# Kernel tuning notes

Measured on AMD Instinct MI355X. Metric: run time of the kernel, lower is better.

## Reference

```python
import jax, jax.numpy as jnp
import numpy as np

N = 50000          # nodes
E = 800000         # edges (avg degree 16)
HID = 128          # hidden_dim
NUM_RBF = 32
CUTOFF = 6.0
LIGAND_NODE = 0
D_IN = 3 * HID + NUM_RBF + 1  # 417


def setup_inputs() -> dict:
    key = jax.random.key(0)
    ks = jax.random.split(key, 16)
    s = 0.05
    return {
        "h": jax.random.normal(ks[0], (N, HID), dtype=jnp.float32),
        "pos": jax.random.normal(ks[1], (N, 3), dtype=jnp.float32) * 3.0,
        "edge_index": jax.random.randint(ks[2], (2, E), 0, N, dtype=jnp.int32),
        "edge_type": jax.random.randint(ks[3], (E,), 0, 2, dtype=jnp.int32),
        "node_type": jax.random.randint(ks[4], (N,), 0, 2, dtype=jnp.int32),
        "emb": jax.random.normal(ks[5], (2, HID), dtype=jnp.float32) * s,
        "mw1": jax.random.normal(ks[6], (D_IN, HID), dtype=jnp.float32) * s,
        "mb1": jnp.zeros((HID,), dtype=jnp.float32),
        "mw2": jax.random.normal(ks[7], (HID, HID), dtype=jnp.float32) * s,
        "mb2": jnp.zeros((HID,), dtype=jnp.float32),
        "uw1": jax.random.normal(ks[8], (2 * HID, HID), dtype=jnp.float32) * s,
        "ub1": jnp.zeros((HID,), dtype=jnp.float32),
        "uw2": jax.random.normal(ks[9], (HID, HID), dtype=jnp.float32) * s,
        "ub2": jnp.zeros((HID,), dtype=jnp.float32),
        "ln_g": jnp.ones((HID,), dtype=jnp.float32),
        "ln_b": jnp.zeros((HID,), dtype=jnp.float32),
    }


def _silu(x):
    return x * jax.nn.sigmoid(x)


def _layernorm(x, g, b, eps=1e-5):
    mu = jnp.mean(x, axis=-1, keepdims=True)
    var = jnp.var(x, axis=-1, keepdims=True)
    return (x - mu) * jax.lax.rsqrt(var + eps) * g + b


def reference(h, pos, edge_index, edge_type, node_type,
              emb, mw1, mb1, mw2, mb2, uw1, ub1, uw2, ub2, ln_g, ln_b):
    # Gaussian RBF setup (matches torch.linspace(0, cutoff, num_rbf))
    centers = jnp.linspace(0.0, CUTOFF, NUM_RBF)          # [R]
    step = CUTOFF / (NUM_RBF - 1)
    gamma = 1.0 / max(step * step, 1e-6)

    src, dst = edge_index[0], edge_index[1]               # [E]
    rel = pos[src] - pos[dst]                             # [E,3]
    dist = jnp.linalg.norm(rel, axis=-1)                  # [E]
    radial = jnp.exp(-gamma * (dist[:, None] - centers[None, :]) ** 2)  # [E,R]
    edge_kind = emb[edge_type]                            # [E,H]

    # edge message MLP (dropout in eval mode = identity)
    m_in = jnp.concatenate([h[src], h[dst], edge_kind, radial, dist[:, None]], axis=-1)  # [E, 3H+R+1]
    x = _silu(m_in @ mw1 + mb1)
    messages = _silu(x @ mw2 + mb2)                       # [E,H]

    # scatter-mean over dst into N nodes
    sums = jax.ops.segment_sum(messages, dst, num_segments=N)           # [N,H]
    counts = jax.ops.segment_sum(jnp.ones((E,), dtype=h.dtype), dst, num_segments=N)
    aggregated = sums / jnp.maximum(counts, 1.0)[:, None]

    # node update MLP
    u = _silu(jnp.concatenate([h, aggregated], axis=-1) @ uw1 + ub1)
    update = u @ uw2 + ub2                                # [N,H]

    # masked residual + LayerNorm (only ligand nodes updated)
    normed = _layernorm(h + update, ln_g, ln_b)
    ligand_mask = (node_type == LIGAND_NODE)[:, None]
    return jnp.where(ligand_mask, normed, h)
```

## Files before the change

kernel.cpp:

```cpp
#include <hip/hip_runtime.h>
#include <hip/hip_bf16.h>
#include <math.h>

#define NN   50000
#define NE   800000
#define HID  128
#define NRBF 32
#define NSCAN_BLOCKS ((NN + 255) / 256)

typedef __attribute__((ext_vector_type(8))) short short8;
typedef __attribute__((ext_vector_type(4))) float floatx4;

constexpr int TILE_N = 64;

__device__ __forceinline__ float silu_f(float x) {
  return x / (1.0f + __expf(-x));
}
__device__ __forceinline__ ushort f2bf(float f) {
  __hip_bfloat16 b = __float2bfloat16(f);
  return *reinterpret_cast<ushort*>(&b);
}
__device__ __forceinline__ float bf2f(ushort u) {
  union { uint u32; float f; } c; c.u32 = ((uint)u) << 16; return c.f;
}

__global__ void counts_i_kernel(const int* __restrict__ edge_index, int* __restrict__ cnt) {
  const int e = blockIdx.x * blockDim.x + threadIdx.x;
  if (e < NE) atomicAdd(&cnt[edge_index[NE + e]], 1);
}

__global__ void scan_a_kernel(const int* __restrict__ cnt, int* __restrict__ incl,
                              int* __restrict__ bsum) {
  __shared__ int s[256];
  const int i = blockIdx.x * 256 + threadIdx.x;
  const int v = (i < NN) ? cnt[i] : 0;
  s[threadIdx.x] = v;
  __syncthreads();
  for (int off = 1; off < 256; off <<= 1) {
    const int x = (threadIdx.x >= off) ? s[threadIdx.x - off] : 0;
    __syncthreads();
    s[threadIdx.x] += x;
    __syncthreads();
  }
  if (i < NN) incl[i] = s[threadIdx.x];
  if (threadIdx.x == 255) bsum[blockIdx.x] = s[255];
}

__global__ void scan_b_kernel(int* __restrict__ bsum, int nb) {
  __shared__ int s[256];
  const int v = (threadIdx.x < nb) ? bsum[threadIdx.x] : 0;
  s[threadIdx.x] = v;
  __syncthreads();
  for (int off = 1; off < 256; off <<= 1) {
    const int x = (threadIdx.x >= off) ? s[threadIdx.x - off] : 0;
    __syncthreads();
    s[threadIdx.x] += x;
    __syncthreads();
  }
  bsum[threadIdx.x] = s[threadIdx.x] - v;
}

__global__ void scan_c_kernel(int* __restrict__ incl, const int* __restrict__ cnt,
                              const int* __restrict__ bsumex, float* __restrict__ cf) {
  const int i = blockIdx.x * 256 + threadIdx.x;
  if (i < NN) {
    const int c = cnt[i];
    incl[i] = incl[i] - c + bsumex[blockIdx.x];
    cf[i] = (float)c;
  }
}

__global__ void perm_kernel(const int* __restrict__ edge_index, const int* __restrict__ edge_type,
                            const int* __restrict__ starts,
                            int* __restrict__ cursor, int2* __restrict__ rec) {
  const int e = blockIdx.x * blockDim.x + threadIdx.x;
  if (e < NE) {
    const int s  = edge_index[e];
    const int d  = edge_index[NE + e];
    const int et = edge_type[e];
    const int pos = atomicAdd(&cursor[d], 1);
    rec[starts[d] + pos] = make_int2(s | (et << 24), d);
  }
}

__global__ void embp_kernel(const float* __restrict__ emb, const float* __restrict__ mw1,
                            const float* __restrict__ mb1, float* __restrict__ embp) {
  const int t = threadIdx.x;
  const int row = t >> 7, col = t & 127;
  float s = mb1[col];
  #pragma unroll 4
  for (int k = 0; k < HID; ++k)
    s = fmaf(emb[row * HID + k], mw1[(256 + k) * HID + col], s);
  embp[row * HID + col] = s;
}

__global__ void pack_w_kernel(const float* __restrict__ W, ushort* __restrict__ out,
                              int Korig, int nks) {
  const int tid = blockIdx.x * blockDim.x + threadIdx.x;
  if (tid >= nks * 8 * 64) return;
  const int l = tid & 63;
  const int c = (tid >> 6) & 7;
  const int kk = tid >> 9;
  union { ushort u[8]; uint4 v; } o;
  #pragma unroll
  for (int j = 0; j < 8; ++j) {
    const int k = kk * 32 + ((l >> 4) * 8) + j;
    const float f = (k < Korig) ? W[k * HID + c * 16 + (l & 15)] : 0.0f;
    o.u[j] = f2bf(f);
  }
  reinterpret_cast<uint4*>(out)[tid] = o.v;
}

__global__ __launch_bounds__(256, 3)
void proj_kernel(const float* __restrict__ h,
                 const ushort* __restrict__ wap, const ushort* __restrict__ wbp,
                 ushort* __restrict__ hs_proj, ushort* __restrict__ hd_proj)
{
  __shared__ __align__(16) ushort sH[64 * HID];
  char* const sHb = reinterpret_cast<char*>(sH);
  const int t  = threadIdx.x;
  const int n0 = blockIdx.x * 64;

  {
    const int e = t >> 2, c0 = (t & 3) * 32;
    const int node = n0 + e;
    const int sm = (e & 7) << 4;
    #pragma unroll
    for (int m = 0; m < 4; ++m) {
      const int c = c0 + m * 8;
      float4 f0 = make_float4(0,0,0,0), f1 = f0;
      if (node < NN) {
        f0 = *reinterpret_cast<const float4*>(h + (long)node * HID + c);
        f1 = *reinterpret_cast<const float4*>(h + (long)node * HID + c + 4);
      }
      union { ushort u[8]; uint4 v; } o;
      o.u[0]=f2bf(f0.x); o.u[1]=f2bf(f0.y); o.u[2]=f2bf(f0.z); o.u[3]=f2bf(f0.w);
      o.u[4]=f2bf(f1.x); o.u[5]=f2bf(f1.y); o.u[6]=f2bf(f1.z); o.u[7]=f2bf(f1.w);
      *reinterpret_cast<uint4*>(sHb + ((e * 256 + c * 2) ^ sm)) = o.v;
    }
  }
  __syncthreads();

  const int lane = t & 63;
  const int w    = t >> 6;
  const int rt0  = (w & 1) * 2;
  const int ct0  = (w >> 1) * 4;
  const int lrow = lane & 15;
  const int lk16 = (lane >> 4) * 16;
  const int rowA0 = rt0 * 16 + lrow, rowA1 = rowA0 + 16;
  const int smA0 = (rowA0 & 7) << 4, smA1 = (rowA1 & 7) << 4;

  floatx4 accA[2][4] = {}, accB[2][4] = {};
  const ushort* const baseA = wap + ((size_t)ct0 * 64 + lane) * 8;
  const ushort* const baseB = wbp + ((size_t)ct0 * 64 + lane) * 8;
  #pragma unroll
  for (int kk = 0; kk < 4; ++kk) {
    short8 afr[2];
    afr[0] = *reinterpret_cast<const short8*>(sHb + rowA0 * 256 + ((kk*64 + lk16) ^ smA0));
    afr[1] = *reinterpret_cast<const short8*>(sHb + rowA1 * 256 + ((kk*64 + lk16) ^ smA1));
    #pragma unroll
    for (int j = 0; j < 4; ++j) {
      const short8 bA = *reinterpret_cast<const short8*>(baseA + kk * 4096 + j * 512);
      const short8 bB = *reinterpret_cast<const short8*>(baseB + kk * 4096 + j * 512);
      #pragma unroll
      for (int i = 0; i < 2; ++i) {
        accA[i][j] = __builtin_amdgcn_mfma_f32_16x16x32_bf16(afr[i], bA, accA[i][j], 0, 0, 0);
        accB[i][j] = __builtin_amdgcn_mfma_f32_16x16x32_bf16(afr[i], bB, accB[i][j], 0, 0, 0);
      }
    }
  }
  #pragma unroll
  for (int i = 0; i < 2; ++i)
    #pragma unroll
    for (int r = 0; r < 4; ++r) {
      const int row = (rt0 + i) * 16 + (lane >> 4) * 4 + r;
      const int node = n0 + row;
      if (node < NN) {
        #pragma unroll
        for (int j = 0; j < 4; ++j) {
          const int col = (ct0 + j) * 16 + lrow;
          hs_proj[(long)node * HID + col] = f2bf(accA[i][j][r]);
          hd_proj[(long)node * HID + col] = f2bf(accB[i][j][r]);
        }
      }
    }
}

__global__ __launch_bounds__(256, 4)
void edge_kernel(const ushort* __restrict__ hs_proj, const ushort* __restrict__ hd_proj,
                 const float* __restrict__ pos, const int2* __restrict__ rec,
                 const float* __restrict__ embp, const float* __restrict__ w416,
                 const ushort* __restrict__ w1dp, const ushort* __restrict__ w2p,
                 const float* __restrict__ mb2,
                 float* sums)
{
  __shared__ __align__(16) uint4 sRbf[64 * 4];
  __shared__ __align__(16) char  sBuf[64 * 512];
  __shared__ int sDst[64];

  const int t  = threadIdx.x;
  const int e0 = blockIdx.x * 64;
  const int e  = t >> 2, q = t & 3;

  const int2 rc = rec[e0 + e];
  const int src = rc.x & 0x00FFFFFF;
  const int et  = ((unsigned)rc.x) >> 24;
  const int dst = rc.y;
  if (q == 0) sDst[e] = dst;

  const float dx = pos[3*src]   - pos[3*dst];
  const float dy = pos[3*src+1] - pos[3*dst+1];
  const float dz = pos[3*src+2] - pos[3*dst+2];
  const float dist = sqrtf(dx*dx + dy*dy + dz*dz);

  {
    const int c0 = q * 32;
    const ushort* const hsr = hs_proj + (long)src * HID;
    const ushort* const hdr = hd_proj + (long)dst * HID;
    const float*  const ep  = embp + et * HID;
    const int sm = (e & 7) << 4;
    #pragma unroll
    for (int m = 0; m < 4; ++m) {
      const int c = c0 + m * 8;
      const uint4 a = *reinterpret_cast<const uint4*>(hsr + c);
      const uint4 b = *reinterpret_cast<const uint4*>(hdr + c);
      const float4 ef0 = *reinterpret_cast<const float4*>(ep + c);
      const float4 ef1 = *reinterpret_cast<const float4*>(ep + c + 4);
      const float4 w0  = *reinterpret_cast<const float4*>(w416 + c);
      const float4 w1  = *reinterpret_cast<const float4*>(w416 + c + 4);
      const ushort* au = reinterpret_cast<const ushort*>(&a);
      const ushort* bu = reinterpret_cast<const ushort*>(&b);
      float4 o0, o1;
      o0.x = bf2f(au[0]) + bf2f(bu[0]) + ef0.x + dist * w0.x;
      o0.y = bf2f(au[1]) + bf2f(bu[1]) + ef0.y + dist * w0.y;
      o0.z = bf2f(au[2]) + bf2f(bu[2]) + ef0.z + dist * w0.z;
      o0.w = bf2f(au[3]) + bf2f(bu[3]) + ef0.w + dist * w0.w;
      o1.x = bf2f(au[4]) + bf2f(bu[4]) + ef1.x + dist * w1.x;
      o1.y = bf2f(au[5]) + bf2f(bu[5]) + ef1.y + dist * w1.y;
      o1.z = bf2f(au[6]) + bf2f(bu[6]) + ef1.z + dist * w1.z;
      o1.w = bf2f(au[7]) + bf2f(bu[7]) + ef1.w + dist * w1.w;
      const int byte0 = e * 512 + c * 4;
      *reinterpret_cast<float4*>(sBuf + (byte0 ^ sm))        = o0;
      *reinterpret_cast<float4*>(sBuf + ((byte0 + 16) ^ sm)) = o1;
    }
    const float step  = 6.0f / 31.0f;
    const float gamma = 1.0f / (step * step);
    const int r0 = q * 8;
    union { ushort u[8]; uint4 v; } o;
    #pragma unroll
    for (int j = 0; j < 8; ++j) {
      const float dd = dist - step * (float)(r0 + j);
      o.u[j] = f2bf(__expf(-gamma * dd * dd));
    }
    sRbf[e * 4 + (q ^ (e & 3))] = o.v;
  }
  __syncthreads();

  const int lane = t & 63;
  const int w    = t >> 6;
  const int rt0  = (w & 1) * 2;
  const int ct0  = (w >> 1) * 4;
  const int lrow = lane & 15;
  const int lk16 = (lane >> 4) * 16;
  const int rowA0 = rt0 * 16 + lrow, rowA1 = rowA0 + 16;
  const int smA0 = (rowA0 & 7) << 4, smA1 = (rowA1 & 7) << 4;

  floatx4 acc[2][4];
  #pragma unroll
  for (int i = 0; i < 2; ++i)
    #pragma unroll
    for (int r = 0; r < 4; ++r) {
      const int row = (rt0 + i) * 16 + (lane >> 4) * 4 + r;
      const int sm = (row & 7) << 4;
      #pragma unroll
      for (int j = 0; j < 4; ++j) {
        const int col = (ct0 + j) * 16 + lrow;
        acc[i][j][r] = *reinterpret_cast<const float*>(sBuf + ((row * 512 + col * 4) ^ sm));
      }
    }
  {
    short8 a0 = *reinterpret_cast<const short8*>(&sRbf[rowA0 * 4 + ((lane >> 4) ^ (rowA0 & 3))]);
    short8 a1 = *reinterpret_cast<const short8*>(&sRbf[rowA1 * 4 + ((lane >> 4) ^ (rowA1 & 3))]);
    #pragma unroll
    for (int j = 0; j < 4; ++j) {
      const short8 b = *reinterpret_cast<const short8*>(w1dp + ((size_t)(ct0 + j) * 64 + lane) * 8);
      acc[0][j] = __builtin_amdgcn_mfma_f32_16x16x32_bf16(a0, b, acc[0][j], 0, 0, 0);
      acc[1][j] = __builtin_amdgcn_mfma_f32_16x16x32_bf16(a1, b, acc[1][j], 0, 0, 0);
    }
  }
  __syncthreads();

  #pragma unroll
  for (int i = 0; i < 2; ++i)
    #pragma unroll
    for (int r = 0; r < 4; ++r) {
      const int row = (rt0 + i) * 16 + (lane >> 4) * 4 + r;
      const int sm = (row & 7) << 4;
      #pragma unroll
      for (int j = 0; j < 4; ++j) {
        const int col = (ct0 + j) * 16 + lrow;
        *reinterpret_cast<ushort*>(sBuf + row * 256 + ((col * 2) ^ sm)) = f2bf(silu_f(acc[i][j][r]));
      }
    }
  __syncthreads();

  floatx4 acc2[2][4] = {};
  {
    const ushort* const bbase = w2p + ((size_t)ct0 * 64 + lane) * 8;
    #pragma unroll 2
    for (int kk = 0; kk < 4; ++kk) {
      short8 bfr[4];
      #pragma unroll
      for (int j = 0; j < 4; ++j)
        bfr[j] = *reinterpret_cast<const short8*>(bbase + kk * 4096 + j * 512);
      short8 afr[2];
      afr[0] = *reinterpret_cast<const short8*>(sBuf + rowA0 * 256 + ((kk*64 + lk16) ^ smA0));
      afr[1] = *reinterpret_cast<const short8*>(sBuf + rowA1 * 256 + ((kk*64 + lk16) ^ smA1));
      #pragma unroll
      for (int i = 0; i < 2; ++i)
        #pragma unroll
        for (int j = 0; j < 4; ++j)
          acc2[i][j] = __builtin_amdgcn_mfma_f32_16x16x32_bf16(afr[i], bfr[j], acc2[i][j], 0, 0, 0);
    }
  }
  __syncthreads();

  {
    float b2v[4];
    #pragma unroll
    for (int j = 0; j < 4; ++j) b2v[j] = mb2[(ct0 + j) * 16 + lrow];
    #pragma unroll
    for (int i = 0; i < 2; ++i)
      #pragma unroll
      for (int r = 0; r < 4; ++r) {
        const int row = (rt0 + i) * 16 + (lane >> 4) * 4 + r;
        const int sm = (row & 7) << 4;
        #pragma unroll
        for (int j = 0; j < 4; ++j) {
          const int col = (ct0 + j) * 16 + lrow;
          *reinterpret_cast<float*>(sBuf + ((row * 512 + col * 4) ^ sm)) =
              silu_f(acc2[i][j][r] + b2v[j]);
        }
      }
  }
  __syncthreads();

  {
    const int half = t >> 7;
    const int c    = t & 127;
    const int r0   = half * 32;
    int cur = sDst[r0];
    float accv = 0.0f;
    for (int r = r0; r < r0 + 32; ++r) {
      const int d = sDst[r];
      const float mv = *reinterpret_cast<const float*>(
          sBuf + ((r * 512 + c * 4) ^ ((r & 7) << 4)));
      if (d != cur) {
        atomicAdd(&sums[(long)cur * HID + c], accv);
        accv = 0.0f;
        cur = d;
      }
      accv += mv;
    }
    atomicAdd(&sums[(long)cur * HID + c], accv);
  }
}

__global__ __launch_bounds__(256, 2)
void node_kernel(const float* __restrict__ h,
                 const float* sums, const float* __restrict__ counts,
                 const int* __restrict__ node_type,
                 const float* __restrict__ uw1, const float* __restrict__ ub1,
                 const float* __restrict__ uw2, const float* __restrict__ ub2,
                 const float* __restrict__ ln_g, const float* __restrict__ ln_b,
                 float* out)
{
  __shared__ float sIn[TILE_N * 256];
  __shared__ float sMu[TILE_N];
  __shared__ float sRs[TILE_N];

  const int t  = threadIdx.x;
  const int n0 = blockIdx.x * TILE_N;

  for (int idx = t; idx < TILE_N*HID; idx += 256) {
    const int n = idx >> 7, c = idx & (HID-1);
    const int node = n0 + n;
    float hv = 0.f, av = 0.f;
    if (node < NN) {
      hv = h[(long)node*HID + c];
      av = sums[(long)node*HID + c] / fmaxf(counts[node], 1.0f);
    }
    sIn[n*256 + c]       = hv;
    sIn[n*256 + HID + c] = av;
  }
  __syncthreads();

  const int tx = t & 31;
  const int ty = t >> 5;

  const float* wp = uw1 + tx*4;
  float4 acc[8];
  #pragma unroll
  for (int i = 0; i < 8; ++i) acc[i] = make_float4(0.f,0.f,0.f,0.f);
  for (int k = 0; k < 2*HID; ++k) {
    const float4 w = *reinterpret_cast<const float4*>(wp + (long)k*HID);
    #pragma unroll
    for (int i = 0; i < 8; ++i) {
      const float a = sIn[(ty*8+i)*256 + k];
      acc[i].x = fmaf(a, w.x, acc[i].x);
      acc[i].y = fmaf(a, w.y, acc[i].y);
      acc[i].z = fmaf(a, w.z, acc[i].z);
      acc[i].w = fmaf(a, w.w, acc[i].w);
    }
  }
  __syncthreads();

  const float4 b1 = *reinterpret_cast<const float4*>(ub1 + tx*4);
  #pragma unroll
  for (int i = 0; i < 8; ++i) {
    const int e = ty*8 + i;
    float4 v = acc[i];
    v.x = silu_f(v.x + b1.x); v.y = silu_f(v.y + b1.y);
    v.z = silu_f(v.z + b1.z); v.w = silu_f(v.w + b1.w);
    *reinterpret_cast<float4*>(&sIn[e*256 + HID + tx*4]) = v;
  }
  __syncthreads();

  const float* wp2 = uw2 + tx*4;
  float4 acc2[8];
  #pragma unroll
  for (int i = 0; i < 8; ++i) acc2[i] = make_float4(0.f,0.f,0.f,0.f);
  for (int k = 0; k < HID; ++k) {
    const float4 w = *reinterpret_cast<const float4*>(wp2 + (long)k*HID);
    #pragma unroll
    for (int i = 0; i < 8; ++i) {
      const float a = sIn[(ty*8+i)*256 + HID + k];
      acc2[i].x = fmaf(a, w.x, acc2[i].x);
      acc2[i].y = fmaf(a, w.y, acc2[i].y);
      acc2[i].z = fmaf(a, w.z, acc2[i].z);
      acc2[i].w = fmaf(a, w.w, acc2[i].w);
    }
  }
  __syncthreads();

  const float4 b2 = *reinterpret_cast<const float4*>(ub2 + tx*4);
  #pragma unroll
  for (int i = 0; i < 8; ++i) {
    const int e = ty*8 + i;
    float4 v = acc2[i];
    v.x = sIn[e*256 + tx*4+0] + v.x + b2.x;
    v.y = sIn[e*256 + tx*4+1] + v.y + b2.y;
    v.z = sIn[e*256 + tx*4+2] + v.z + b2.z;
    v.w = sIn[e*256 + tx*4+3] + v.w + b2.w;
    *reinterpret_cast<float4*>(&sIn[e*256 + HID + tx*4]) = v;
  }
  __syncthreads();

  {
    const int n = t >> 2, q = t & 3;
    float sm = 0.f, sq = 0.f;
    #pragma unroll 8
    for (int i = 0; i < 32; ++i) {
      const float v = sIn[n*256 + HID + q*32 + i];
      sm += v; sq += v*v;
    }
    sm += __shfl_xor(sm, 1); sq += __shfl_xor(sq, 1);
    sm += __shfl_xor(sm, 2); sq += __shfl_xor(sq, 2);
    const float mu  = sm * (1.0f/HID);
    float var = sq * (1.0f/HID) - mu*mu;
    var = fmaxf(var, 0.0f);
    if (q == 0) { sMu[n] = mu; sRs[n] = rsqrtf(var + 1e-5f); }
  }
  __syncthreads();

  for (int idx = t; idx < TILE_N*HID; idx += 256) {
    const int n = idx >> 7, c = idx & (HID-1);
    const int node = n0 + n;
    if (node >= NN) continue;
    const float xv = sIn[n*256 + HID + c];
    const float normed = (xv - sMu[n]) * sRs[n] * ln_g[c] + ln_b[c];
    const float hv = sIn[n*256 + c];
    out[(long)node*HID + c] = (node_type[node] == 0) ? normed : hv;
  }
}

extern "C" void kernel_launch(void* const* d_in, const int* in_sizes, int n_in,
                              void* d_out, int out_size, void* d_ws, size_t ws_size,
                              hipStream_t stream)
{
  const float* h    = (const float*)d_in[0];
  const float* pos  = (const float*)d_in[1];
  const int*   eidx = (const int*)  d_in[2];
  const int*   etyp = (const int*)  d_in[3];
  const int*   ntyp = (const int*)  d_in[4];
  const float* emb  = (const float*)d_in[5];
  const float* mw1  = (const float*)d_in[6];
  const float* mb1  = (const float*)d_in[7];
  const float* mw2  = (const float*)d_in[8];
  const float* mb2  = (const float*)d_in[9];
  const float* uw1  = (const float*)d_in[10];
  const float* ub1  = (const float*)d_in[11];
  const float* uw2  = (const float*)d_in[12];
  const float* ub2  = (const float*)d_in[13];
  const float* lng  = (const float*)d_in[14];
  const float* lnb  = (const float*)d_in[15];

  float* sums = (float*)d_out;

  float*  counts_f = (float*)d_ws;
  ushort* hs_proj  = (ushort*)(counts_f + NN);
  ushort* hd_proj  = hs_proj + (long)NN*HID;
  float*  embp     = (float*)(hd_proj + (long)NN*HID);
  ushort* wap      = (ushort*)(embp + 256);
  ushort* wbp      = wap + 4*4096;
  ushort* w1dp     = wbp + 4*4096;
  ushort* w2p      = w1dp + 1*4096;
  int*    cnt_i    = (int*)(w2p + 4*4096);
  int*    cursor   = cnt_i + NN;
  int*    starts   = cursor + NN;
  int*    bsum     = starts + NN;
  int2*   rec      = (int2*)(bsum + 256);

  hipMemsetAsync(sums, 0, (size_t)NN*HID*4, stream);
  hipMemsetAsync(cnt_i, 0, (size_t)NN*2*4, stream);

  counts_i_kernel<<<(NE + 255)/256, 256, 0, stream>>>(eidx, cnt_i);
  scan_a_kernel<<<NSCAN_BLOCKS, 256, 0, stream>>>(cnt_i, starts, bsum);
  scan_b_kernel<<<1, 256, 0, stream>>>(bsum, NSCAN_BLOCKS);
  scan_c_kernel<<<NSCAN_BLOCKS, 256, 0, stream>>>(starts, cnt_i, bsum, counts_f);
  perm_kernel<<<(NE + 255)/256, 256, 0, stream>>>(eidx, etyp, starts, cursor, rec);

  embp_kernel<<<1, 256, 0, stream>>>(emb, mw1, mb1, embp);
  pack_w_kernel<<<8,  256, 0, stream>>>(mw1,             wap,  128, 4);
  pack_w_kernel<<<8,  256, 0, stream>>>(mw1 + 128*HID,   wbp,  128, 4);
  pack_w_kernel<<<2,  256, 0, stream>>>(mw1 + 384*HID,   w1dp,  32, 1);
  pack_w_kernel<<<8,  256, 0, stream>>>(mw2,             w2p,  128, 4);

  proj_kernel<<<(NN + 63)/64, 256, 0, stream>>>(h, wap, wbp, hs_proj, hd_proj);
  edge_kernel<<<NE/64, 256, 0, stream>>>(hs_proj, hd_proj, pos, rec,
                                         embp, mw1 + 416*HID, w1dp, w2p, mb2, sums);
  node_kernel<<<(NN + 63)/64, 256, 0, stream>>>(h, sums, counts_f, ntyp,
                                                uw1, ub1, uw2, ub2,
                                                lng, lnb, (float*)d_out);
}
```

Before: 447.5 us.

## Shrink edge kernel LDS via bf16 staging and fold dist/embedding terms into MFMA

The edge kernel now stages the summed projections and the final messages in shared memory as bf16 instead of fp32, which cuts LDS from about 49KB to about 20KB per block. Launch bounds rise from 4 to 7 blocks per CU. The dist*w416 and edge-type embedding contributions are moved out of per-element FMAs and into an extra K=32 MFMA step, using one-hot edge-type columns and a packed extra weight block built by a new prep kernel. In exchange, precision drops from rounding the pre-activation sums, dist and the messages to bf16, and there is one extra MFMA pass per tile.

Measured after the change: 533.4 us. 19.2% more time.

```diff
diff --git a/kernel.cpp b/kernel.cpp
--- a/kernel.cpp
+++ b/kernel.cpp
@@ -94,6 +94,19 @@
   embp[row * HID + col] = s;
 }
 
+__global__ void build_w1x_kernel(const float* __restrict__ mw1, const float* __restrict__ embp,
+                                 float* __restrict__ w1x) {
+  const int tid = blockIdx.x * 256 + threadIdx.x;
+  if (tid >= 64 * 128) return;
+  const int r = tid >> 7, c = tid & 127;
+  float v = 0.0f;
+  if (r < 32)       v = mw1[(384 + r) * HID + c];
+  else if (r == 32) v = mw1[416 * HID + c];
+  else if (r == 33) v = embp[c];
+  else if (r == 34) v = embp[HID + c];
+  w1x[tid] = v;
+}
+
 __global__ void pack_w_kernel(const float* __restrict__ W, ushort* __restrict__ out,
                               int Korig, int nks) {
   const int tid = blockIdx.x * blockDim.x + threadIdx.x;
@@ -186,17 +199,17 @@
     }
 }
 
-__global__ __launch_bounds__(256, 4)
+__global__ __launch_bounds__(256, 7)
 void edge_kernel(const ushort* __restrict__ hs_proj, const ushort* __restrict__ hd_proj,
                  const float* __restrict__ pos, const int2* __restrict__ rec,
-                 const float* __restrict__ embp, const float* __restrict__ w416,
-                 const ushort* __restrict__ w1dp, const ushort* __restrict__ w2p,
+                 const ushort* __restrict__ w1xp, const ushort* __restrict__ w2p,
                  const float* __restrict__ mb2,
                  float* sums)
 {
-  __shared__ __align__(16) uint4 sRbf[64 * 4];
-  __shared__ __align__(16) char  sBuf[64 * 512];
-  __shared__ int sDst[64];
+  __shared__ __align__(16) char sBuf[20480];
+  __shared__ int   sDst[64];
+  __shared__ int   sEt[64];
+  __shared__ float sDistF[64];
 
   const int t  = threadIdx.x;
   const int e0 = blockIdx.x * 64;
@@ -206,42 +219,28 @@
   const int src = rc.x & 0x00FFFFFF;
   const int et  = ((unsigned)rc.x) >> 24;
   const int dst = rc.y;
-  if (q == 0) sDst[e] = dst;
 
   const float dx = pos[3*src]   - pos[3*dst];
   const float dy = pos[3*src+1] - pos[3*dst+1];
   const float dz = pos[3*src+2] - pos[3*dst+2];
   const float dist = sqrtf(dx*dx + dy*dy + dz*dz);
-
-  {
-    const int c0 = q * 32;
+  if (q == 0) { sDst[e] = dst; sEt[e] = et; sDistF[e] = dist; }
+
+  {
     const ushort* const hsr = hs_proj + (long)src * HID;
     const ushort* const hdr = hd_proj + (long)dst * HID;
-    const float*  const ep  = embp + et * HID;
     const int sm = (e & 7) << 4;
     #pragma unroll
     for (int m = 0; m < 4; ++m) {
-      const int c = c0 + m * 8;
+      const int c = q * 32 + m * 8;
       const uint4 a = *reinterpret_cast<const uint4*>(hsr + c);
       const uint4 b = *reinterpret_cast<const uint4*>(hdr + c);
-      const float4 ef0 = *reinterpret_cast<const float4*>(ep + c);
-      const float4 ef1 = *reinterpret_cast<const float4*>(ep + c + 4);
-      const float4 w0  = *reinterpret_cast<const float4*>(w416 + c);
-      const float4 w1  = *reinterpret_cast<const float4*>(w416 + c + 4);
       const ushort* au = reinterpret_cast<const ushort*>(&a);
       const ushort* bu = reinterpret_cast<const ushort*>(&b);
-      float4 o0, o1;
-      o0.x = bf2f(au[0]) + bf2f(bu[0]) + ef0.x + dist * w0.x;
-      o0.y = bf2f(au[1]) + bf2f(bu[1]) + ef0.y + dist * w0.y;
-      o0.z = bf2f(au[2]) + bf2f(bu[2]) + ef0.z + dist * w0.z;
-      o0.w = bf2f(au[3]) + bf2f(bu[3]) + ef0.w + dist * w0.w;
-      o1.x = bf2f(au[4]) + bf2f(bu[4]) + ef1.x + dist * w1.x;
-      o1.y = bf2f(au[5]) + bf2f(bu[5]) + ef1.y + dist * w1.y;
-      o1.z = bf2f(au[6]) + bf2f(bu[6]) + ef1.z + dist * w1.z;
-      o1.w = bf2f(au[7]) + bf2f(bu[7]) + ef1.w + dist * w1.w;
-      const int byte0 = e * 512 + c * 4;
-      *reinterpret_cast<float4*>(sBuf + (byte0 ^ sm))        = o0;
-      *reinterpret_cast<float4*>(sBuf + ((byte0 + 16) ^ sm)) = o1;
+      union { ushort u[8]; uint4 v; } o;
+      #pragma unroll
+      for (int j = 0; j < 8; ++j) o.u[j] = f2bf(bf2f(au[j]) + bf2f(bu[j]));
+      *reinterpret_cast<uint4*>(sBuf + ((e * 256 + c * 2) ^ sm)) = o.v;
     }
     const float step  = 6.0f / 31.0f;
     const float gamma = 1.0f / (step * step);
@@ -252,7 +251,7 @@
       const float dd = dist - step * (float)(r0 + j);
       o.u[j] = f2bf(__expf(-gamma * dd * dd));
     }
-    sRbf[e * 4 + (q ^ (e & 3))] = o.v;
+    reinterpret_cast<uint4*>(sBuf + 16384)[e * 4 + (q ^ (e & 3))] = o.v;
   }
   __syncthreads();
 
@@ -275,20 +274,37 @@
       #pragma unroll
       for (int j = 0; j < 4; ++j) {
         const int col = (ct0 + j) * 16 + lrow;
-        acc[i][j][r] = *reinterpret_cast<const float*>(sBuf + ((row * 512 + col * 4) ^ sm));
-      }
-    }
-  {
-    short8 a0 = *reinterpret_cast<const short8*>(&sRbf[rowA0 * 4 + ((lane >> 4) ^ (rowA0 & 3))]);
-    short8 a1 = *reinterpret_cast<const short8*>(&sRbf[rowA1 * 4 + ((lane >> 4) ^ (rowA1 & 3))]);
+        acc[i][j][r] = bf2f(*reinterpret_cast<const ushort*>(
+            sBuf + row * 256 + ((col * 2) ^ sm)));
+      }
+    }
+  {
+    const uint4* const sRbf = reinterpret_cast<const uint4*>(sBuf + 16384);
+    const short8 a0 = *reinterpret_cast<const short8*>(&sRbf[rowA0 * 4 + ((lane >> 4) ^ (rowA0 & 3))]);
+    const short8 a1 = *reinterpret_cast<const short8*>(&sRbf[rowA1 * 4 + ((lane >> 4) ^ (rowA1 & 3))]);
+    const ushort* const bb = w1xp + ((size_t)ct0 * 64 + lane) * 8;
     #pragma unroll
     for (int j = 0; j < 4; ++j) {
-      const short8 b = *reinterpret_cast<const short8*>(w1dp + ((size_t)(ct0 + j) * 64 + lane) * 8);
+      const short8 b = *reinterpret_cast<const short8*>(bb + j * 512);
       acc[0][j] = __builtin_amdgcn_mfma_f32_16x16x32_bf16(a0, b, acc[0][j], 0, 0, 0);
       acc[1][j] = __builtin_amdgcn_mfma_f32_16x16x32_bf16(a1, b, acc[1][j], 0, 0, 0);
     }
-  }
-  __syncthreads();
+    short8 x0 = {0,0,0,0,0,0,0,0}, x1 = {0,0,0,0,0,0,0,0};
+    if ((lane >> 4) == 0) {
+      x0[0] = (short)f2bf(sDistF[rowA0]);
+      x0[1] = (sEt[rowA0] == 0) ? (short)0x3F80 : (short)0;
+      x0[2] = (sEt[rowA0] == 1) ? (short)0x3F80 : (short)0;
+      x1[0] = (short)f2bf(sDistF[rowA1]);
+      x1[1] = (sEt[rowA1] == 0) ? (short)0x3F80 : (short)0;
+      x1[2] = (sEt[rowA1] == 1) ? (short)0x3F80 : (short)0;
+    }
+    #pragma unroll
+    for (int j = 0; j < 4; ++j) {
+      const short8 b = *reinterpret_cast<const short8*>(bb + 4096 + j * 512);
+      acc[0][j] = __builtin_amdgcn_mfma_f32_16x16x32_bf16(x0, b, acc[0][j], 0, 0, 0);
+      acc[1][j] = __builtin_amdgcn_mfma_f32_16x16x32_bf16(x1, b, acc[1][j], 0, 0, 0);
+    }
+  }
 
   #pragma unroll
   for (int i = 0; i < 2; ++i)
@@ -299,7 +315,8 @@
       #pragma unroll
       for (int j = 0; j < 4; ++j) {
         const int col = (ct0 + j) * 16 + lrow;
-        *reinterpret_cast<ushort*>(sBuf + row * 256 + ((col * 2) ^ sm)) = f2bf(silu_f(acc[i][j][r]));
+        *reinterpret_cast<ushort*>(sBuf + row * 256 + ((col * 2) ^ sm)) =
+            f2bf(silu_f(acc[i][j][r]));
       }
     }
   __syncthreads();
@@ -338,8 +355,8 @@
         #pragma unroll
         for (int j = 0; j < 4; ++j) {
           const int col = (ct0 + j) * 16 + lrow;
-          *reinterpret_cast<float*>(sBuf + ((row * 512 + col * 4) ^ sm)) =
-              silu_f(acc2[i][j][r] + b2v[j]);
+          *reinterpret_cast<ushort*>(sBuf + row * 256 + ((col * 2) ^ sm)) =
+              f2bf(silu_f(acc2[i][j][r] + b2v[j]));
         }
       }
   }
@@ -353,8 +370,8 @@
     float accv = 0.0f;
     for (int r = r0; r < r0 + 32; ++r) {
       const int d = sDst[r];
-      const float mv = *reinterpret_cast<const float*>(
-          sBuf + ((r * 512 + c * 4) ^ ((r & 7) << 4)));
+      const float mv = bf2f(*reinterpret_cast<const ushort*>(
+          sBuf + r * 256 + ((c * 2) ^ ((r & 7) << 4))));
       if (d != cur) {
         atomicAdd(&sums[(long)cur * HID + c], accv);
         accv = 0.0f;
@@ -511,10 +528,11 @@
   ushort* hs_proj  = (ushort*)(counts_f + NN);
   ushort* hd_proj  = hs_proj + (long)NN*HID;
   float*  embp     = (float*)(hd_proj + (long)NN*HID);
-  ushort* wap      = (ushort*)(embp + 256);
+  float*  w1x      = embp + 256;
+  ushort* wap      = (ushort*)(w1x + 64*128);
   ushort* wbp      = wap + 4*4096;
-  ushort* w1dp     = wbp + 4*4096;
-  ushort* w2p      = w1dp + 1*4096;
+  ushort* w1xp     = wbp + 4*4096;
+  ushort* w2p      = w1xp + 2*4096;
   int*    cnt_i    = (int*)(w2p + 4*4096);
   int*    cursor   = cnt_i + NN;
   int*    starts   = cursor + NN;
@@ -531,14 +549,15 @@
   perm_kernel<<<(NE + 255)/256, 256, 0, stream>>>(eidx, etyp, starts, cursor, rec);
 
   embp_kernel<<<1, 256, 0, stream>>>(emb, mw1, mb1, embp);
-  pack_w_kernel<<<8,  256, 0, stream>>>(mw1,             wap,  128, 4);
-  pack_w_kernel<<<8,  256, 0, stream>>>(mw1 + 128*HID,   wbp,  128, 4);
-  pack_w_kernel<<<2,  256, 0, stream>>>(mw1 + 384*HID,   w1dp,  32, 1);
-  pack_w_kernel<<<8,  256, 0, stream>>>(mw2,             w2p,  128, 4);
+  build_w1x_kernel<<<32, 256, 0, stream>>>(mw1, embp, w1x);
+  pack_w_kernel<<<8, 256, 0, stream>>>(mw1,           wap,  128, 4);
+  pack_w_kernel<<<8, 256, 0, stream>>>(mw1 + 128*HID, wbp,  128, 4);
+  pack_w_kernel<<<4, 256, 0, stream>>>(w1x,           w1xp,  64, 2);
+  pack_w_kernel<<<8, 256, 0, stream>>>(mw2,           w2p,  128, 4);
 
   proj_kernel<<<(NN + 63)/64, 256, 0, stream>>>(h, wap, wbp, hs_proj, hd_proj);
   edge_kernel<<<NE/64, 256, 0, stream>>>(hs_proj, hd_proj, pos, rec,
-                                         embp, mw1 + 416*HID, w1dp, w2p, mb2, sums);
+                                         w1xp, w2p, mb2, sums);
   node_kernel<<<(NN + 63)/64, 256, 0, stream>>>(h, sums, counts_f, ntyp,
                                                 uw1, ub1, uw2, ub2,
                                                 lng, lnb, (float*)d_out);
```
